# Kernel optimization log

Measured on AMD Instinct MI355X. Metric: run time of the kernel, lower is better.

The kernel has to match this reference:

```python
import jax, jax.numpy as jnp
import numpy as np

NUM_HEADS = 16
HEAD_SIZE = 64
N_EMBD = 1024


def setup_inputs() -> dict:
    key = jax.random.key(0)
    ks = jax.random.split(key, 6)
    B, T, C = 2, 2048, N_EMBD
    scale = 0.02
    return {
        "x": jax.random.normal(ks[0], (B, T, C), dtype=jnp.float32),
        "Wq": jax.random.normal(ks[1], (C, NUM_HEADS * HEAD_SIZE), dtype=jnp.float32) * scale,
        "Wk": jax.random.normal(ks[2], (C, NUM_HEADS * HEAD_SIZE), dtype=jnp.float32) * scale,
        "Wv": jax.random.normal(ks[3], (C, NUM_HEADS * HEAD_SIZE), dtype=jnp.float32) * scale,
        "Wo": jax.random.normal(ks[4], (NUM_HEADS * HEAD_SIZE, C), dtype=jnp.float32) * scale,
        "bo": jnp.zeros((C,), dtype=jnp.float32),
    }


def reference(x, Wq, Wk, Wv, Wo, bo):
    B, T, C = x.shape
    H, D = NUM_HEADS, HEAD_SIZE
    # QKV projections (no bias), reshape to [B, H, T, D]
    q = (x @ Wq).reshape(B, T, H, D).transpose(0, 2, 1, 3)
    k = (x @ Wk).reshape(B, T, H, D).transpose(0, 2, 1, 3)
    v = (x @ Wv).reshape(B, T, H, D).transpose(0, 2, 1, 3)
    # scaled dot-product scores [B, H, T, T]
    scores = jnp.einsum("bhqd,bhkd->bhqk", q, k) / jnp.sqrt(jnp.float32(D))
    causal = jnp.tril(jnp.ones((T, T), dtype=bool))
    scores = jnp.where(causal, scores, -jnp.inf)
    weights = jax.nn.softmax(scores, axis=-1)  # dropout = identity (eval)
    out = jnp.einsum("bhqk,bhkd->bhqd", weights, v)
    out = out.transpose(0, 2, 1, 3).reshape(B, T, H * D)
    return out @ Wo + bo
```

## Files before the change

### kernel.cpp

```cpp
#include <hip/hip_runtime.h>

typedef __attribute__((ext_vector_type(8))) _Float16 f16x8;
typedef __attribute__((ext_vector_type(4))) _Float16 f16x4;
typedef __attribute__((ext_vector_type(2))) _Float16 f16x2;
typedef __attribute__((ext_vector_type(2))) __fp16   fp16x2_raw;
typedef __attribute__((ext_vector_type(4))) float    f32x4;

#define NUM_HEADS 16
#define HEAD_D 64
#define EMB 1024
#define SEQ 2048
#define BATCH 2
#define MTOT (BATCH * SEQ)

#define QALPHA 0.18033688011112042f

__device__ __forceinline__ f16x2 cvt_pk_f16(float lo, float hi)
{
    fp16x2_raw r = __builtin_amdgcn_cvt_pkrtz(lo, hi);
    return __builtin_bit_cast(f16x2, r);
}

#if defined(__has_builtin)
#if __has_builtin(__builtin_amdgcn_exp2f)
#define HAVE_EXP2 1
#endif
#endif
__device__ __forceinline__ float fast_exp2(float x)
{
#ifdef HAVE_EXP2
    return __builtin_amdgcn_exp2f(x);
#else
    return __expf(x * 0.6931471805599453f);
#endif
}

#if defined(__has_builtin)
#if __has_builtin(__builtin_amdgcn_global_load_lds)
#define HAVE_GLOAD_LDS 1
#endif
#endif

__device__ __forceinline__ void stage16(const void* g, void* ldsWaveBase, int lane)
{
#ifdef HAVE_GLOAD_LDS
    __builtin_amdgcn_global_load_lds(
        (const __attribute__((address_space(1))) void*)g,
        (__attribute__((address_space(3))) void*)ldsWaveBase, 16, 0, 0);
    (void)lane;
#else
    *(f16x8*)((char*)ldsWaveBase + lane * 16) = *(const f16x8*)g;
#endif
}

__global__ __launch_bounds__(256) void prep_all(
    const float* __restrict__ x,
    const float* __restrict__ Wq, const float* __restrict__ Wk,
    const float* __restrict__ Wv, const float* __restrict__ Wo,
    _Float16* __restrict__ xh, _Float16* __restrict__ Wt,
    _Float16* __restrict__ Wto)
{
    const int z = blockIdx.z;
    if (z == 4) {
        int base = ((blockIdx.y * 32 + blockIdx.x) * 256 + threadIdx.x) * 2;
        #pragma unroll
        for (int t = 0; t < 2; ++t) {
            int i = base + t;
            float4 a = ((const float4*)x)[i * 2];
            float4 b = ((const float4*)x)[i * 2 + 1];
            f16x8 o;
            o[0] = (_Float16)a.x; o[1] = (_Float16)a.y;
            o[2] = (_Float16)a.z; o[3] = (_Float16)a.w;
            o[4] = (_Float16)b.x; o[5] = (_Float16)b.y;
            o[6] = (_Float16)b.z; o[7] = (_Float16)b.w;
            ((f16x8*)xh)[i] = o;
        }
        return;
    }
    const float* W = z == 0 ? Wq : (z == 1 ? Wk : (z == 2 ? Wv : Wo));
    _Float16* D = (z == 3) ? Wto : (Wt + (size_t)z * EMB * EMB);
    __shared__ float tile[32][33];
    const int tx = threadIdx.x & 31, ty = threadIdx.x >> 5;
    const int n0 = blockIdx.x * 32, k0 = blockIdx.y * 32;
    #pragma unroll
    for (int j = 0; j < 4; ++j)
        tile[ty + j * 8][tx] = W[(size_t)(k0 + ty + j * 8) * EMB + n0 + tx];
    __syncthreads();
    #pragma unroll
    for (int j = 0; j < 4; ++j)
        D[(size_t)(n0 + ty + j * 8) * EMB + k0 + tx] =
            (_Float16)tile[tx][ty + j * 8];
}

template <int MODE>
__global__ __launch_bounds__(256) void gemm_mfma(
    const _Float16* __restrict__ A, const _Float16* __restrict__ Bt,
    _Float16* __restrict__ Qh, _Float16* __restrict__ Kh,
    _Float16* __restrict__ Vh,
    float* __restrict__ outf, const float* __restrict__ bias)
{
    __shared__ __align__(16) _Float16 As[128 * 32];
    __shared__ __align__(16) _Float16 Bs[128 * 32];

    const int tid = threadIdx.x;
    const int w = tid >> 6, lane = tid & 63;
    const int l15 = lane & 15, g4 = lane >> 4;
    const int wm = w >> 1, wn = w & 1;
    const int row0 = blockIdx.y * 128, col0 = blockIdx.x * 128;

    f32x4 acc[4][4];
    #pragma unroll
    for (int mt = 0; mt < 4; ++mt)
        #pragma unroll
        for (int nt = 0; nt < 4; ++nt)
            acc[mt][nt] = (f32x4){0.f, 0.f, 0.f, 0.f};

    for (int k0 = 0; k0 < EMB; k0 += 32) {
        __syncthreads();
        #pragma unroll
        for (int i = 0; i < 2; ++i) {
            int c = (i << 8) + tid;
            int row = c >> 2, u = c & 3;
            stage16(&A[(size_t)(row0 + row) * EMB + k0 + (u << 3)],
                    (char*)As + (i << 12) + (w << 10), lane);
            stage16(&Bt[(size_t)(col0 + row) * EMB + k0 + (u << 3)],
                    (char*)Bs + (i << 12) + (w << 10), lane);
        }
        __syncthreads();

        f16x8 af[4], bf[4];
        #pragma unroll
        for (int mt = 0; mt < 4; ++mt)
            af[mt] = *(const f16x8*)((const char*)As +
                     ((wm << 6) + (mt << 4) + l15) * 64 + (g4 << 4));
        #pragma unroll
        for (int nt = 0; nt < 4; ++nt)
            bf[nt] = *(const f16x8*)((const char*)Bs +
                     ((wn << 6) + (nt << 4) + l15) * 64 + (g4 << 4));
        #pragma unroll
        for (int mt = 0; mt < 4; ++mt)
            #pragma unroll
            for (int nt = 0; nt < 4; ++nt)
                acc[mt][nt] = __builtin_amdgcn_mfma_f32_16x16x32_f16(
                    af[mt], bf[nt], acc[mt][nt], 0, 0, 0);
    }

    #pragma unroll
    for (int mt = 0; mt < 4; ++mt) {
        int m = row0 + (wm << 6) + (mt << 4) + (g4 << 2);
        #pragma unroll
        for (int nt = 0; nt < 4; ++nt) {
            int gcol = col0 + (wn << 6) + (nt << 4) + l15;
            if (MODE == 0) {
                int proj = gcol >> 10, pc = gcol & 1023;
                int h = pc >> 6, d = pc & 63;
                _Float16* dst = proj == 0 ? Qh : (proj == 1 ? Kh : Vh);
                float alpha = proj == 0 ? QALPHA : 1.0f;
                int b = m >> 11, t = m & 2047;
                #pragma unroll
                for (int r = 0; r < 4; ++r)
                    dst[(((size_t)(b * NUM_HEADS + h)) * SEQ + t + r) * HEAD_D + d] =
                        (_Float16)(acc[mt][nt][r] * alpha);
            } else {
                float bz = bias[gcol];
                #pragma unroll
                for (int r = 0; r < 4; ++r)
                    outf[(size_t)(m + r) * EMB + gcol] = acc[mt][nt][r] + bz;
            }
        }
    }
}

__device__ __forceinline__ void attn_tile(
    const char* __restrict__ KsC, const char* __restrict__ VtC,
    char* __restrict__ pwv,
    f16x8 qf0, f16x8 qf1, f32x4 (&acc)[4], float& m, float& l,
    bool diag, int qrel, int l15, int g)
{
    f32x4 st[4];
    #pragma unroll
    for (int nt = 0; nt < 4; ++nt) {
        int kvl = (nt << 4) + l15;
        f16x8 kf0 = *(const f16x8*)&KsC[kvl * 128 + (((g << 4)) ^ ((kvl & 7) << 4))];
        f16x8 kf1 = *(const f16x8*)&KsC[kvl * 128 + ((64 + (g << 4)) ^ ((kvl & 7) << 4))];
        f32x4 z = (f32x4){0.f, 0.f, 0.f, 0.f};
        z = __builtin_amdgcn_mfma_f32_16x16x32_f16(kf0, qf0, z, 0, 0, 0);
        z = __builtin_amdgcn_mfma_f32_16x16x32_f16(kf1, qf1, z, 0, 0, 0);
        st[nt] = z;
    }
    if (diag) {
        #pragma unroll
        for (int nt = 0; nt < 4; ++nt)
            #pragma unroll
            for (int r = 0; r < 4; ++r)
                if ((nt << 4) + (g << 2) + r > qrel) st[nt][r] = -1e30f;
    }

    float mx;
    {
        float a0 = fmaxf(fmaxf(st[0][0], st[0][1]), fmaxf(st[0][2], st[0][3]));
        float a1 = fmaxf(fmaxf(st[1][0], st[1][1]), fmaxf(st[1][2], st[1][3]));
        float a2 = fmaxf(fmaxf(st[2][0], st[2][1]), fmaxf(st[2][2], st[2][3]));
        float a3 = fmaxf(fmaxf(st[3][0], st[3][1]), fmaxf(st[3][2], st[3][3]));
        mx = fmaxf(fmaxf(a0, a1), fmaxf(a2, a3));
    }
    mx = fmaxf(mx, __shfl_xor(mx, 16));
    mx = fmaxf(mx, __shfl_xor(mx, 32));

    if (!__all(mx - m <= 8.0f)) {
        float nm = fmaxf(m, mx);
        float sc = fast_exp2(m - nm);
        m = nm;
        l *= sc;
        #pragma unroll
        for (int r = 0; r < 4; ++r) {
            float scr = __shfl(sc, (g << 2) + r);
            acc[0][r] *= scr; acc[1][r] *= scr;
            acc[2][r] *= scr; acc[3][r] *= scr;
        }
    }

    float ps = 0.f;
    #pragma unroll
    for (int nt = 0; nt < 4; ++nt)
        #pragma unroll
        for (int r = 0; r < 4; ++r) {
            float p = fast_exp2(st[nt][r] - m);
            st[nt][r] = p;
            ps += p;
        }
    ps += __shfl_xor(ps, 16);
    ps += __shfl_xor(ps, 32);
    l += ps;

    #pragma unroll
    for (int nt = 0; nt < 4; ++nt)
        #pragma unroll
        for (int rr = 0; rr < 2; ++rr) {
            int kvb = (nt << 4) + (g << 2) + (rr << 1);
            f16x2 pv = cvt_pk_f16(st[nt][rr * 2], st[nt][rr * 2 + 1]);
            *(f16x2*)&pwv[l15 * 128 + ((kvb << 1) ^ ((l15 & 7) << 4))] = pv;
        }
    f16x8 pa0 = *(const f16x8*)&pwv[l15 * 128 + (((g << 4)) ^ ((l15 & 7) << 4))];
    f16x8 pa1 = *(const f16x8*)&pwv[l15 * 128 + ((64 + (g << 4)) ^ ((l15 & 7) << 4))];

    #pragma unroll
    for (int dn = 0; dn < 4; ++dn) {
        int d = (dn << 4) + l15;
        int swz = ((d & 7) ^ (d >> 3)) & 7;
        f16x8 vf0 = *(const f16x8*)&VtC[d * 128 + (((g << 4)) ^ (swz << 4))];
        f16x8 vf1 = *(const f16x8*)&VtC[d * 128 + ((64 + (g << 4)) ^ (swz << 4))];
        acc[dn] = __builtin_amdgcn_mfma_f32_16x16x32_f16(pa0, vf0, acc[dn], 0, 0, 0);
        acc[dn] = __builtin_amdgcn_mfma_f32_16x16x32_f16(pa1, vf1, acc[dn], 0, 0, 0);
    }
}

__global__ __launch_bounds__(256) void attn_mfma(
    const _Float16* __restrict__ Qh, const _Float16* __restrict__ Kh,
    const _Float16* __restrict__ Vh, _Float16* __restrict__ O)
{
    __shared__ char lds[48 * 1024];

    const int qtA = blockIdx.x;
    const int qtB = (SEQ / 64 - 1) - qtA;
    const int bh = blockIdx.y;
    const int q0A = qtA << 6, q0B = qtB << 6;
    const int tid = threadIdx.x;
    const int w = tid >> 6, lane = tid & 63;
    const int l15 = lane & 15, g = lane >> 4;

    const size_t headbase = (size_t)bh * SEQ * HEAD_D;

    const int qrowA = q0A + (w << 4) + l15;
    const int qrowB = q0B + (w << 4) + l15;
    f16x8 qfA0 = *(const f16x8*)&Qh[headbase + (size_t)qrowA * HEAD_D + (g << 3)];
    f16x8 qfA1 = *(const f16x8*)&Qh[headbase + (size_t)qrowA * HEAD_D + 32 + (g << 3)];
    f16x8 qfB0 = *(const f16x8*)&Qh[headbase + (size_t)qrowB * HEAD_D + (g << 3)];
    f16x8 qfB1 = *(const f16x8*)&Qh[headbase + (size_t)qrowB * HEAD_D + 32 + (g << 3)];

    f32x4 accA[4], accB[4];
    #pragma unroll
    for (int dn = 0; dn < 4; ++dn) {
        accA[dn] = (f32x4){0.f, 0.f, 0.f, 0.f};
        accB[dn] = (f32x4){0.f, 0.f, 0.f, 0.f};
    }
    float mA = -1e30f, lA = 0.f, mB = -1e30f, lB = 0.f;

    const int c0 = tid, c1 = 256 + tid;
    const int row_a = c0 >> 3, u_a = c0 & 7;
    const int row_b = c1 >> 3, u_b = c1 & 7;

    {
        f16x8 k8a = *(const f16x8*)&Kh[headbase + (size_t)row_a * HEAD_D + (u_a << 3)];
        f16x8 v8a = *(const f16x8*)&Vh[headbase + (size_t)row_a * HEAD_D + (u_a << 3)];
        f16x8 k8b = *(const f16x8*)&Kh[headbase + (size_t)row_b * HEAD_D + (u_b << 3)];
        f16x8 v8b = *(const f16x8*)&Vh[headbase + (size_t)row_b * HEAD_D + (u_b << 3)];
        char* Ks0 = lds;
        char* Vt0 = lds + 16384;
        *(f16x8*)&Ks0[row_a * 128 + ((u_a ^ (row_a & 7)) << 4)] = k8a;
        *(f16x8*)&Ks0[row_b * 128 + ((u_b ^ (row_b & 7)) << 4)] = k8b;
        #pragma unroll
        for (int j = 0; j < 8; ++j) {
            int da = (u_a << 3) + j, db = (u_b << 3) + j;
            *(_Float16*)&Vt0[da * 128 +
                ((row_a << 1) ^ ((((da & 7) ^ (da >> 3)) & 7) << 4))] = v8a[j];
            *(_Float16*)&Vt0[db * 128 +
                ((row_b << 1) ^ ((((db & 7) ^ (db >> 3)) & 7) << 4))] = v8b[j];
        }
    }
    __syncthreads();

    char* pwvA = lds + 32768 + (w << 11);
    char* pwvB = lds + 40960 + (w << 11);

    int cur = 0;
    for (int kt = 0; kt <= qtB; ++kt) {
        const bool have_next = (kt < qtB);

        f16x8 k8a, v8a, k8b, v8b;
        if (have_next) {
            const size_t nb = headbase + (size_t)((kt + 1) << 6) * HEAD_D;
            k8a = *(const f16x8*)&Kh[nb + (size_t)row_a * HEAD_D + (u_a << 3)];
            v8a = *(const f16x8*)&Vh[nb + (size_t)row_a * HEAD_D + (u_a << 3)];
            k8b = *(const f16x8*)&Kh[nb + (size_t)row_b * HEAD_D + (u_b << 3)];
            v8b = *(const f16x8*)&Vh[nb + (size_t)row_b * HEAD_D + (u_b << 3)];
        }

        const char* KsC = lds + (cur << 13);
        const char* VtC = lds + 16384 + (cur << 13);
        const int qrel = (w << 4) + l15;

        if (kt <= qtA) {
            attn_tile(KsC, VtC, pwvA, qfA0, qfA1, accA, mA, lA,
                      kt == qtA, qrel, l15, g);
            attn_tile(KsC, VtC, pwvB, qfB0, qfB1, accB, mB, lB,
                      false, qrel, l15, g);
        } else {
            attn_tile(KsC, VtC, pwvB, qfB0, qfB1, accB, mB, lB,
                      kt == qtB, qrel, l15, g);
        }

        if (have_next) {
            char* KsN = lds + ((cur ^ 1) << 13);
            char* VtN = lds + 16384 + ((cur ^ 1) << 13);
            *(f16x8*)&KsN[row_a * 128 + ((u_a ^ (row_a & 7)) << 4)] = k8a;
            *(f16x8*)&KsN[row_b * 128 + ((u_b ^ (row_b & 7)) << 4)] = k8b;
            #pragma unroll
            for (int j = 0; j < 8; ++j) {
                int da = (u_a << 3) + j, db = (u_b << 3) + j;
                *(_Float16*)&VtN[da * 128 +
                    ((row_a << 1) ^ ((((da & 7) ^ (da >> 3)) & 7) << 4))] = v8a[j];
                *(_Float16*)&VtN[db * 128 +
                    ((row_b << 1) ^ ((((db & 7) ^ (db >> 3)) & 7) << 4))] = v8b[j];
            }
        }
        __syncthreads();
        cur ^= 1;
    }

    const int b = bh >> 4, h = bh & 15;
    const float rlA = 1.f / lA, rlB = 1.f / lB;
    #pragma unroll
    for (int r = 0; r < 4; ++r) {
        float invA = __shfl(rlA, (g << 2) + r);
        float invB = __shfl(rlB, (g << 2) + r);
        int tokA = (b << 11) + q0A + (w << 4) + (g << 2) + r;
        int tokB = (b << 11) + q0B + (w << 4) + (g << 2) + r;
        #pragma unroll
        for (int dn = 0; dn < 4; ++dn) {
            O[(size_t)tokA * EMB + (h << 6) + (dn << 4) + l15] =
                (_Float16)(accA[dn][r] * invA);
            O[(size_t)tokB * EMB + (h << 6) + (dn << 4) + l15] =
                (_Float16)(accB[dn][r] * invB);
        }
    }
}

extern "C" void kernel_launch(void* const* d_in, const int* in_sizes, int n_in,
                              void* d_out, int out_size, void* d_ws, size_t ws_size,
                              hipStream_t stream)
{
    const float* x  = (const float*)d_in[0];
    const float* Wq = (const float*)d_in[1];
    const float* Wk = (const float*)d_in[2];
    const float* Wv = (const float*)d_in[3];
    const float* Wo = (const float*)d_in[4];
    const float* bo = (const float*)d_in[5];
    float* out = (float*)d_out;

    const size_t ME = (size_t)MTOT * EMB;
    const size_t WE = (size_t)EMB * EMB;
    const size_t need = (ME + 3 * WE + WE + 3 * ME + ME) * sizeof(_Float16);
    if (ws_size < need) return;

    _Float16* xh  = (_Float16*)d_ws;
    _Float16* Wt  = xh + ME;
    _Float16* Wto = Wt + 3 * WE;
    _Float16* Qh  = Wto + WE;
    _Float16* Kh  = Qh + ME;
    _Float16* Vh  = Kh + ME;
    _Float16* Ow  = Vh + ME;

    prep_all<<<dim3(EMB / 32, EMB / 32, 5), 256, 0, stream>>>(
        x, Wq, Wk, Wv, Wo, xh, Wt, Wto);

    gemm_mfma<0><<<dim3(3 * EMB / 128, MTOT / 128), 256, 0, stream>>>(
        xh, Wt, Qh, Kh, Vh, nullptr, nullptr);

    attn_mfma<<<dim3(SEQ / 128, BATCH * NUM_HEADS), 256, 0, stream>>>(Qh, Kh, Vh, Ow);

    gemm_mfma<1><<<dim3(EMB / 128, MTOT / 128), 256, 0, stream>>>(
        Ow, Wto, nullptr, nullptr, nullptr, out, bo);
}
```

Before: 128.3 us.

## Pre-transpose V in global memory and stage K/V tiles via async copies

Adds a separate kernel that writes V in a head-dim-major layout, so the attention kernel no longer transposes V with scalar 2-byte LDS stores. K and V tiles are now staged through a stage16 helper (likely a direct global-to-LDS copy), replacing the register round trip of the load-compute-store double buffer. The aim is to cut LDS store cost and register pressure in the attention loop. The price is an extra kernel launch and another full read and write of V in global memory.

```diff
diff --git a/kernel.cpp b/kernel.cpp
--- a/kernel.cpp
+++ b/kernel.cpp
@@ -1,7 +1,6 @@
 #include <hip/hip_runtime.h>
 
 typedef __attribute__((ext_vector_type(8))) _Float16 f16x8;
-typedef __attribute__((ext_vector_type(4))) _Float16 f16x4;
 typedef __attribute__((ext_vector_type(2))) _Float16 f16x2;
 typedef __attribute__((ext_vector_type(2))) __fp16   fp16x2_raw;
 typedef __attribute__((ext_vector_type(4))) float    f32x4;
@@ -90,6 +89,31 @@
     for (int j = 0; j < 4; ++j)
         D[(size_t)(n0 + ty + j * 8) * EMB + k0 + tx] =
             (_Float16)tile[tx][ty + j * 8];
+}
+
+__global__ __launch_bounds__(256) void transpose_v(
+    const _Float16* __restrict__ Vh, _Float16* __restrict__ VhT)
+{
+    __shared__ _Float16 tile[64][72];
+    const int t0 = blockIdx.x << 6, bh = blockIdx.y;
+    const size_t hb  = (size_t)bh * SEQ * HEAD_D;
+    const size_t hb2 = (size_t)bh * HEAD_D * SEQ;
+    const int tid = threadIdx.x;
+    #pragma unroll
+    for (int i = 0; i < 2; ++i) {
+        int c = (i << 8) + tid, row = c >> 3, u = c & 7;
+        f16x8 v = *(const f16x8*)&Vh[hb + (size_t)(t0 + row) * HEAD_D + (u << 3)];
+        #pragma unroll
+        for (int j = 0; j < 8; ++j)
+            tile[(u << 3) + j][row] = v[j];
+    }
+    __syncthreads();
+    #pragma unroll
+    for (int i = 0; i < 2; ++i) {
+        int c = (i << 8) + tid, row = c >> 3, u = c & 7;
+        *(f16x8*)&VhT[hb2 + (size_t)row * SEQ + t0 + (u << 3)] =
+            *(const f16x8*)&tile[row][u << 3];
+    }
 }
 
 template <int MODE>
@@ -171,6 +195,23 @@
     }
 }
 
+__device__ __forceinline__ void stage_kv_tile(
+    const _Float16* __restrict__ KhB, const _Float16* __restrict__ VtB,
+    int kv0, char* __restrict__ KsBuf, char* __restrict__ VtBuf,
+    int w, int lane)
+{
+    #pragma unroll
+    for (int i = 0; i < 2; ++i) {
+        int c = (i << 8) + (w << 6) + lane;
+        int row = c >> 3, u = c & 7;
+        int us = u ^ (row & 7);
+        stage16(&KhB[(size_t)(kv0 + row) * HEAD_D + (us << 3)],
+                KsBuf + (i << 12) + (w << 10), lane);
+        stage16(&VtB[(size_t)row * SEQ + kv0 + (us << 3)],
+                VtBuf + (i << 12) + (w << 10), lane);
+    }
+}
+
 __device__ __forceinline__ void attn_tile(
     const char* __restrict__ KsC, const char* __restrict__ VtC,
     char* __restrict__ pwv,
@@ -247,9 +288,8 @@
     #pragma unroll
     for (int dn = 0; dn < 4; ++dn) {
         int d = (dn << 4) + l15;
-        int swz = ((d & 7) ^ (d >> 3)) & 7;
-        f16x8 vf0 = *(const f16x8*)&VtC[d * 128 + (((g << 4)) ^ (swz << 4))];
-        f16x8 vf1 = *(const f16x8*)&VtC[d * 128 + ((64 + (g << 4)) ^ (swz << 4))];
+        f16x8 vf0 = *(const f16x8*)&VtC[d * 128 + (((g << 4)) ^ ((d & 7) << 4))];
+        f16x8 vf1 = *(const f16x8*)&VtC[d * 128 + ((64 + (g << 4)) ^ ((d & 7) << 4))];
         acc[dn] = __builtin_amdgcn_mfma_f32_16x16x32_f16(pa0, vf0, acc[dn], 0, 0, 0);
         acc[dn] = __builtin_amdgcn_mfma_f32_16x16x32_f16(pa1, vf1, acc[dn], 0, 0, 0);
     }
@@ -257,7 +297,7 @@
 
 __global__ __launch_bounds__(256) void attn_mfma(
     const _Float16* __restrict__ Qh, const _Float16* __restrict__ Kh,
-    const _Float16* __restrict__ Vh, _Float16* __restrict__ O)
+    const _Float16* __restrict__ VhT, _Float16* __restrict__ O)
 {
     __shared__ char lds[48 * 1024];
 
@@ -269,6 +309,8 @@
     const int w = tid >> 6, lane = tid & 63;
     const int l15 = lane & 15, g = lane >> 4;
 
+    const _Float16* KhB = Kh  + (size_t)bh * SEQ * HEAD_D;
+    const _Float16* VtB = VhT + (size_t)bh * HEAD_D * SEQ;
     const size_t headbase = (size_t)bh * SEQ * HEAD_D;
 
     const int qrowA = q0A + (w << 4) + l15;
@@ -286,28 +328,7 @@
     }
     float mA = -1e30f, lA = 0.f, mB = -1e30f, lB = 0.f;
 
-    const int c0 = tid, c1 = 256 + tid;
-    const int row_a = c0 >> 3, u_a = c0 & 7;
-    const int row_b = c1 >> 3, u_b = c1 & 7;
-
-    {
-        f16x8 k8a = *(const f16x8*)&Kh[headbase + (size_t)row_a * HEAD_D + (u_a << 3)];
-        f16x8 v8a = *(const f16x8*)&Vh[headbase + (size_t)row_a * HEAD_D + (u_a << 3)];
-        f16x8 k8b = *(const f16x8*)&Kh[headbase + (size_t)row_b * HEAD_D + (u_b << 3)];
-        f16x8 v8b = *(const f16x8*)&Vh[headbase + (size_t)row_b * HEAD_D + (u_b << 3)];
-        char* Ks0 = lds;
-        char* Vt0 = lds + 16384;
-        *(f16x8*)&Ks0[row_a * 128 + ((u_a ^ (row_a & 7)) << 4)] = k8a;
-        *(f16x8*)&Ks0[row_b * 128 + ((u_b ^ (row_b & 7)) << 4)] = k8b;
-        #pragma unroll
-        for (int j = 0; j < 8; ++j) {
-            int da = (u_a << 3) + j, db = (u_b << 3) + j;
-            *(_Float16*)&Vt0[da * 128 +
-                ((row_a << 1) ^ ((((da & 7) ^ (da >> 3)) & 7) << 4))] = v8a[j];
-            *(_Float16*)&Vt0[db * 128 +
-                ((row_b << 1) ^ ((((db & 7) ^ (db >> 3)) & 7) << 4))] = v8b[j];
-        }
-    }
+    stage_kv_tile(KhB, VtB, 0, lds, lds + 16384, w, lane);
     __syncthreads();
 
     char* pwvA = lds + 32768 + (w << 11);
@@ -315,16 +336,10 @@
 
     int cur = 0;
     for (int kt = 0; kt <= qtB; ++kt) {
-        const bool have_next = (kt < qtB);
-
-        f16x8 k8a, v8a, k8b, v8b;
-        if (have_next) {
-            const size_t nb = headbase + (size_t)((kt + 1) << 6) * HEAD_D;
-            k8a = *(const f16x8*)&Kh[nb + (size_t)row_a * HEAD_D + (u_a << 3)];
-            v8a = *(const f16x8*)&Vh[nb + (size_t)row_a * HEAD_D + (u_a << 3)];
-            k8b = *(const f16x8*)&Kh[nb + (size_t)row_b * HEAD_D + (u_b << 3)];
-            v8b = *(const f16x8*)&Vh[nb + (size_t)row_b * HEAD_D + (u_b << 3)];
-        }
+        if (kt < qtB)
+            stage_kv_tile(KhB, VtB, (kt + 1) << 6,
+                          lds + ((cur ^ 1) << 13),
+                          lds + 16384 + ((cur ^ 1) << 13), w, lane);
 
         const char* KsC = lds + (cur << 13);
         const char* VtC = lds + 16384 + (cur << 13);
@@ -340,20 +355,6 @@
                       kt == qtB, qrel, l15, g);
         }
 
-        if (have_next) {
-            char* KsN = lds + ((cur ^ 1) << 13);
-            char* VtN = lds + 16384 + ((cur ^ 1) << 13);
-            *(f16x8*)&KsN[row_a * 128 + ((u_a ^ (row_a & 7)) << 4)] = k8a;
-            *(f16x8*)&KsN[row_b * 128 + ((u_b ^ (row_b & 7)) << 4)] = k8b;
-            #pragma unroll
-            for (int j = 0; j < 8; ++j) {
-                int da = (u_a << 3) + j, db = (u_b << 3) + j;
-                *(_Float16*)&VtN[da * 128 +
-                    ((row_a << 1) ^ ((((da & 7) ^ (da >> 3)) & 7) << 4))] = v8a[j];
-                *(_Float16*)&VtN[db * 128 +
-                    ((row_b << 1) ^ ((((db & 7) ^ (db >> 3)) & 7) << 4))] = v8b[j];
-            }
-        }
         __syncthreads();
         cur ^= 1;
     }
@@ -390,7 +391,7 @@
 
     const size_t ME = (size_t)MTOT * EMB;
     const size_t WE = (size_t)EMB * EMB;
-    const size_t need = (ME + 3 * WE + WE + 3 * ME + ME) * sizeof(_Float16);
+    const size_t need = (6 * ME + 4 * WE) * sizeof(_Float16);
     if (ws_size < need) return;
 
     _Float16* xh  = (_Float16*)d_ws;
@@ -400,6 +401,7 @@
     _Float16* Kh  = Qh + ME;
     _Float16* Vh  = Kh + ME;
     _Float16* Ow  = Vh + ME;
+    _Float16* VhT = Ow + ME;
 
     prep_all<<<dim3(EMB / 32, EMB / 32, 5), 256, 0, stream>>>(
         x, Wq, Wk, Wv, Wo, xh, Wt, Wto);
@@ -407,7 +409,9 @@
     gemm_mfma<0><<<dim3(3 * EMB / 128, MTOT / 128), 256, 0, stream>>>(
         xh, Wt, Qh, Kh, Vh, nullptr, nullptr);
 
-    attn_mfma<<<dim3(SEQ / 128, BATCH * NUM_HEADS), 256, 0, stream>>>(Qh, Kh, Vh, Ow);
+    transpose_v<<<dim3(SEQ / 64, BATCH * NUM_HEADS), 256, 0, stream>>>(Vh, VhT);
+
+    attn_mfma<<<dim3(SEQ / 128, BATCH * NUM_HEADS), 256, 0, stream>>>(Qh, Kh, VhT, Ow);
 
     gemm_mfma<1><<<dim3(EMB / 128, MTOT / 128), 256, 0, stream>>>(
         Ow, Wto, nullptr, nullptr, nullptr, out, bo);
```

Result: faster. 125.0 us (-2.5%).
